# Kernel optimization log

Hardware: AMD Instinct MI355X
Metric: run time of the kernel (lower is better)

Reference implementation:

```python
import jax, jax.numpy as jnp
import numpy as np

D_MODEL = 1024
N_HEADS = 16
D_K = D_MODEL // N_HEADS


def setup_inputs() -> dict:
    key = jax.random.key(0)
    ks = jax.random.split(key, 9)
    s = 1.0 / np.sqrt(D_MODEL)
    x = jax.random.normal(ks[0], (4, 2048, D_MODEL), dtype=jnp.float32)
    def lin(kw, kb):
        W = jax.random.uniform(kw, (D_MODEL, D_MODEL), jnp.float32, -s, s)
        b = jax.random.uniform(kb, (D_MODEL,), jnp.float32, -s, s)
        return W, b
    w_q, b_q = lin(ks[1], ks[2])
    w_k, b_k = lin(ks[3], ks[4])
    w_v, b_v = lin(ks[5], ks[6])
    w_o, b_o = lin(ks[7], ks[8])
    return {"x": x, "w_q": w_q, "b_q": b_q, "w_k": w_k, "b_k": b_k,
            "w_v": w_v, "b_v": b_v, "w_o": w_o, "b_o": b_o}


def reference(x, w_q, b_q, w_k, b_k, w_v, b_v, w_o, b_o):
    B, S, _ = x.shape
    # projections; nn.Linear computes x @ W^T + b, here W stored as [in, out]
    def proj(W, b):
        return (x @ W + b).reshape(B, S, N_HEADS, D_K).transpose(0, 2, 1, 3)  # [B,H,S,Dk]
    q = proj(w_q, b_q)
    k = proj(w_k, b_k)
    v = proj(w_v, b_v)
    scores = jnp.einsum("bhsd,bhtd->bhst", q, k) / jnp.sqrt(jnp.float32(D_K))
    attn = jax.nn.softmax(scores, axis=-1)  # dropout p=0 -> identity
    ctx = jnp.einsum("bhst,bhtd->bhsd", attn, v)
    ctx = ctx.transpose(0, 2, 1, 3).reshape(B, S, D_MODEL)
    return ctx @ w_o + b_o
```

## Files before the change

### kernel.cpp

```cpp
#include <hip/hip_runtime.h>
#include <stdint.h>

typedef __attribute__((ext_vector_type(8))) short bf8;
typedef __attribute__((ext_vector_type(4))) float f4;
typedef __attribute__((ext_vector_type(16))) float f16v;
typedef __attribute__((ext_vector_type(4))) int i4;
typedef __attribute__((ext_vector_type(2))) int i2;
typedef unsigned short u16;

#define LDK 56

#define GLOAD16(gptr, lptr)                                                        \
    __builtin_amdgcn_global_load_lds((const __attribute__((address_space(1))) void*)(gptr), \
                                     (__attribute__((address_space(3))) void*)(lptr), 16, 0, 0)

static __device__ inline u16 f2bfbits(float f) {
    unsigned u = __float_as_uint(f);
    unsigned r = 0x7FFFu + ((u >> 16) & 1u);
    return (u16)((u + r) >> 16);
}

static __device__ inline int cvtpk(float lo, float hi) {
    int r;
    asm("v_cvt_pk_bf16_f32 %0, %1, %2" : "=v"(r) : "v"(lo), "v"(hi));
    return r;
}

__global__ void cvt_bf16(const float* __restrict__ in, u16* __restrict__ out, int n) {
    int i = (blockIdx.x * 256 + threadIdx.x) * 4;
    if (i < n) {
        float4 v = *(const float4*)(in + i);
        ushort4 o;
        o.x = f2bfbits(v.x); o.y = f2bfbits(v.y);
        o.z = f2bfbits(v.z); o.w = f2bfbits(v.w);
        *(ushort4*)(out + i) = o;
    }
}

__global__ void transpose4(const float* __restrict__ w0, const float* __restrict__ w1,
                           const float* __restrict__ w2, const float* __restrict__ w3,
                           u16* __restrict__ o0, u16* __restrict__ o1,
                           u16* __restrict__ o2, u16* __restrict__ o3) {
    __shared__ float tile[32][33];
    const float* w = blockIdx.z == 0 ? w0 : blockIdx.z == 1 ? w1 : blockIdx.z == 2 ? w2 : w3;
    u16* o = blockIdx.z == 0 ? o0 : blockIdx.z == 1 ? o1 : blockIdx.z == 2 ? o2 : o3;
    int bx = blockIdx.x * 32, by = blockIdx.y * 32;
    int tx = threadIdx.x, ty = threadIdx.y;
#pragma unroll
    for (int r = 0; r < 32; r += 8)
        tile[ty + r][tx] = w[(size_t)(by + ty + r) * 1024 + bx + tx];
    __syncthreads();
#pragma unroll
    for (int r = 0; r < 32; r += 8)
        o[(size_t)(bx + ty + r) * 1024 + by + tx] = f2bfbits(tile[tx][ty + r]);
}

__global__ __launch_bounds__(256) void gemm128(
    const u16* __restrict__ A, const u16* __restrict__ BT,
    const float* __restrict__ bias,
    u16* __restrict__ outb, float* __restrict__ outf, int mode) {
    __shared__ __align__(16) short As[128][LDK];
    __shared__ __align__(16) short Bs[128][LDK];
    const int tid = threadIdx.x;
    const int lane = tid & 63;
    const int l15 = lane & 15, lg = lane >> 4;
    const int wave = tid >> 6;
    const int wm = (wave >> 1) * 64, wn = (wave & 1) * 64;
    const int m0 = blockIdx.x * 128, n0 = blockIdx.y * 128;
    const int srow = tid >> 2;
    const int scol = (tid & 3) * 8;

    f4 acc[4][4] = {};

    for (int k0 = 0; k0 < 1024; k0 += 32) {
        bf8 a0 = *(const bf8*)(A + (size_t)(m0 + srow) * 1024 + k0 + scol);
        bf8 a1 = *(const bf8*)(A + (size_t)(m0 + srow + 64) * 1024 + k0 + scol);
        bf8 b0 = *(const bf8*)(BT + (size_t)(n0 + srow) * 1024 + k0 + scol);
        bf8 b1 = *(const bf8*)(BT + (size_t)(n0 + srow + 64) * 1024 + k0 + scol);
        __syncthreads();
        *(bf8*)(&As[srow][scol]) = a0;
        *(bf8*)(&As[srow + 64][scol]) = a1;
        *(bf8*)(&Bs[srow][scol]) = b0;
        *(bf8*)(&Bs[srow + 64][scol]) = b1;
        __syncthreads();
        bf8 af[4], bfr[4];
#pragma unroll
        for (int i = 0; i < 4; ++i) af[i] = *(const bf8*)(&As[wm + i * 16 + l15][lg * 8]);
#pragma unroll
        for (int j = 0; j < 4; ++j) bfr[j] = *(const bf8*)(&Bs[wn + j * 16 + l15][lg * 8]);
#pragma unroll
        for (int i = 0; i < 4; ++i)
#pragma unroll
            for (int j = 0; j < 4; ++j)
                acc[i][j] = __builtin_amdgcn_mfma_f32_16x16x32_bf16(af[i], bfr[j], acc[i][j], 0, 0, 0);
    }

    float bj[4];
#pragma unroll
    for (int j = 0; j < 4; ++j) bj[j] = bias[n0 + wn + j * 16 + l15];
    const float sc = (mode == 2) ? 0.125f * 1.44269504088896340736f : 1.0f;

    if (mode == 1) {
#pragma unroll
        for (int i = 0; i < 4; ++i) {
            int gm = m0 + wm + i * 16 + lg * 4;
#pragma unroll
            for (int j = 0; j < 4; ++j) {
                int gn = n0 + wn + j * 16 + l15;
#pragma unroll
                for (int r = 0; r < 4; ++r)
                    outf[(size_t)(gm + r) * 1024 + gn] = acc[i][j][r] + bj[j];
            }
        }
    } else if (mode == 3) {
#pragma unroll
        for (int i = 0; i < 4; ++i) {
            int gm = m0 + wm + i * 16 + lg * 4;
            int b_ = gm >> 11, s0 = gm & 2047;
#pragma unroll
            for (int j = 0; j < 4; ++j) {
                int gn = n0 + wn + j * 16 + l15;
                int h = gn >> 6, d = gn & 63;
                ushort4 w;
                w.x = f2bfbits(acc[i][j][0] + bj[j]);
                w.y = f2bfbits(acc[i][j][1] + bj[j]);
                w.z = f2bfbits(acc[i][j][2] + bj[j]);
                w.w = f2bfbits(acc[i][j][3] + bj[j]);
                *(ushort4*)(outb + ((size_t)(b_ * 16 + h) * 64 + d) * 2048 + s0) = w;
            }
        }
    } else {
#pragma unroll
        for (int i = 0; i < 4; ++i) {
            int gm = m0 + wm + i * 16 + lg * 4;
#pragma unroll
            for (int j = 0; j < 4; ++j) {
                int gn = n0 + wn + j * 16 + l15;
                int h = gn >> 6, d = gn & 63;
#pragma unroll
                for (int r = 0; r < 4; ++r) {
                    int m = gm + r;
                    int b_ = m >> 11, s = m & 2047;
                    float vv = (acc[i][j][r] + bj[j]) * sc;
                    outb[(((size_t)(b_ * 16 + h) * 2048) + s) * 64 + d] = f2bfbits(vv);
                }
            }
        }
    }
}

static __device__ inline void softmax_pv(f16v s, float& l,
                                         f16v& ocA, f16v& ocB, const bf8* vf) {
    float s0 = 0.f, s1 = 0.f, s2 = 0.f, s3 = 0.f;
#pragma unroll
    for (int r = 0; r < 16; r += 4) {
        s[r + 0] = __builtin_amdgcn_exp2f(s[r + 0]); s0 += s[r + 0];
        s[r + 1] = __builtin_amdgcn_exp2f(s[r + 1]); s1 += s[r + 1];
        s[r + 2] = __builtin_amdgcn_exp2f(s[r + 2]); s2 += s[r + 2];
        s[r + 3] = __builtin_amdgcn_exp2f(s[r + 3]); s3 += s[r + 3];
    }
    float ps = (s0 + s1) + (s2 + s3);
    {
        i2 sw = __builtin_amdgcn_permlane32_swap(__float_as_int(ps), __float_as_int(ps), false, false);
        ps = __int_as_float(sw[0]) + __int_as_float(sw[1]);
    }
    l += ps;

    i4 w0, w1;
    {
        i2 r0 = __builtin_amdgcn_permlane32_swap(cvtpk(s[0], s[1]),   cvtpk(s[4], s[5]),   false, false);
        i2 r1 = __builtin_amdgcn_permlane32_swap(cvtpk(s[2], s[3]),   cvtpk(s[6], s[7]),   false, false);
        i2 r2 = __builtin_amdgcn_permlane32_swap(cvtpk(s[8], s[9]),   cvtpk(s[12], s[13]), false, false);
        i2 r3 = __builtin_amdgcn_permlane32_swap(cvtpk(s[10], s[11]), cvtpk(s[14], s[15]), false, false);
        w0[0] = r0[0]; w0[1] = r1[0]; w0[2] = r0[1]; w0[3] = r1[1];
        w1[0] = r2[0]; w1[1] = r3[0]; w1[2] = r2[1]; w1[3] = r3[1];
    }
    union { i4 i; bf8 h; } pa0, pa1;
    pa0.i = w0; pa1.i = w1;

    __builtin_amdgcn_s_setprio(1);
    ocA = __builtin_amdgcn_mfma_f32_32x32x16_bf16(vf[0], pa0.h, ocA, 0, 0, 0);
    ocB = __builtin_amdgcn_mfma_f32_32x32x16_bf16(vf[2], pa0.h, ocB, 0, 0, 0);
    ocA = __builtin_amdgcn_mfma_f32_32x32x16_bf16(vf[1], pa1.h, ocA, 0, 0, 0);
    ocB = __builtin_amdgcn_mfma_f32_32x32x16_bf16(vf[3], pa1.h, ocB, 0, 0, 0);
    __builtin_amdgcn_s_setprio(0);
}

__global__ __launch_bounds__(256, 4) void attn(
    const u16* __restrict__ Q, const u16* __restrict__ K, const u16* __restrict__ VT,
    u16* __restrict__ ctx) {
    __shared__ __align__(16) char Kl[2][8192];
    __shared__ __align__(16) char Vl[2][8192];

    const int tid = threadIdx.x;
    const int lane = tid & 63, wave = tid >> 6;
    const int l31 = lane & 31, hi = lane >> 5;

    const int g = blockIdx.x;
    const int xcd = g & 7, li = g >> 3;
    const int bh = xcd * 8 + (li >> 4);
    const int qblk = li & 15;
    const int q0 = qblk * 128 + wave * 32;

    const char* Kg = (const char*)(K + (size_t)bh * 2048 * 64);
    const char* Vg = (const char*)(VT + (size_t)bh * 64 * 2048);

    const int p0 = wave * 1024 + lane * 16;
    const int p1 = p0 + 4096;
    const int r0 = p0 >> 7, r1 = p1 >> 7;
    const int sc0 = (p0 & 127) ^ ((r0 & 7) << 4);
    const int sc1 = (p1 & 127) ^ ((r1 & 7) << 4);

    GLOAD16(Kg + (size_t)r0 * 128 + sc0, &Kl[0][wave * 1024]);
    GLOAD16(Kg + (size_t)r1 * 128 + sc1, &Kl[0][4096 + wave * 1024]);
    GLOAD16(Vg + (size_t)r0 * 4096 + sc0, &Vl[0][wave * 1024]);
    GLOAD16(Vg + (size_t)r1 * 4096 + sc1, &Vl[0][4096 + wave * 1024]);

    bf8 qf[4];
    {
        const u16* Qr = Q + ((size_t)bh * 2048 + q0 + l31) * 64 + hi * 8;
#pragma unroll
        for (int c = 0; c < 4; ++c) qf[c] = *(const bf8*)(Qr + c * 16);
    }

    f16v oc0 = {}, oc1 = {};
    float l = 0.f;
    const int sw = (l31 & 7) << 4;

    __syncthreads();

    int cur = 0;
    for (int it = 0; it < 32; ++it) {
        const int t0 = it * 64;
        if (it + 1 < 32) {
            const int nxt = cur ^ 1;
            const size_t tn = (size_t)(t0 + 64);
            GLOAD16(Kg + (tn + r0) * 128 + sc0, &Kl[nxt][wave * 1024]);
            GLOAD16(Kg + (tn + r1) * 128 + sc1, &Kl[nxt][4096 + wave * 1024]);
            GLOAD16(Vg + (size_t)r0 * 4096 + tn * 2 + sc0, &Vl[nxt][wave * 1024]);
            GLOAD16(Vg + (size_t)r1 * 4096 + tn * 2 + sc1, &Vl[nxt][4096 + wave * 1024]);
        }
        const char* Kb = Kl[cur];
        const char* Vb = Vl[cur];

#pragma unroll
        for (int st = 0; st < 2; ++st) {
            bf8 kf[4];
#pragma unroll
            for (int c = 0; c < 4; ++c)
                kf[c] = *(const bf8*)(Kb + (st * 32 + l31) * 128 + ((c * 32 + hi * 16) ^ sw));

            f16v s;
#pragma unroll
            for (int r = 0; r < 16; ++r) s[r] = -10.f;
            __builtin_amdgcn_s_setprio(1);
#pragma unroll
            for (int c = 0; c < 4; ++c)
                s = __builtin_amdgcn_mfma_f32_32x32x16_bf16(kf[c], qf[c], s, 0, 0, 0);
            __builtin_amdgcn_s_setprio(0);

            bf8 vf[4];
#pragma unroll
            for (int dt = 0; dt < 2; ++dt)
#pragma unroll
                for (int tc = 0; tc < 2; ++tc)
                    vf[dt * 2 + tc] = *(const bf8*)(Vb + (dt * 32 + l31) * 128 +
                                                    ((st * 64 + tc * 32 + hi * 16) ^ sw));

            softmax_pv(s, l, oc0, oc1, vf);
        }
        __syncthreads();
        cur ^= 1;
    }

    const int b_ = bh >> 4, hd = bh & 15;
    const float rl = __builtin_amdgcn_rcpf(l);
    u16* Cr = ctx + ((size_t)(b_ * 2048) + q0 + l31) * 1024 + hd * 64;
#pragma unroll
    for (int gi = 0; gi < 4; ++gi) {
        ushort4 w;
        w.x = f2bfbits(oc0[gi * 4 + 0] * rl);
        w.y = f2bfbits(oc0[gi * 4 + 1] * rl);
        w.z = f2bfbits(oc0[gi * 4 + 2] * rl);
        w.w = f2bfbits(oc0[gi * 4 + 3] * rl);
        *(ushort4*)(Cr + gi * 8 + hi * 4) = w;
    }
#pragma unroll
    for (int gi = 0; gi < 4; ++gi) {
        ushort4 w;
        w.x = f2bfbits(oc1[gi * 4 + 0] * rl);
        w.y = f2bfbits(oc1[gi * 4 + 1] * rl);
        w.z = f2bfbits(oc1[gi * 4 + 2] * rl);
        w.w = f2bfbits(oc1[gi * 4 + 3] * rl);
        *(ushort4*)(Cr + 32 + gi * 8 + hi * 4) = w;
    }
}

extern "C" void kernel_launch(void* const* d_in, const int* in_sizes, int n_in,
                              void* d_out, int out_size, void* d_ws, size_t ws_size,
                              hipStream_t stream) {
    const float* x  = (const float*)d_in[0];
    const float* wq = (const float*)d_in[1];
    const float* bq = (const float*)d_in[2];
    const float* wk = (const float*)d_in[3];
    const float* bk = (const float*)d_in[4];
    const float* wv = (const float*)d_in[5];
    const float* bv = (const float*)d_in[6];
    const float* wo = (const float*)d_in[7];
    const float* bo = (const float*)d_in[8];
    float* out = (float*)d_out;

    char* ws = (char*)d_ws;
    u16* xb  = (u16*)ws;
    u16* wtq = (u16*)(ws + (size_t)(16 << 20));
    u16* wtk = wtq + 1024 * 1024;
    u16* wtv = wtk + 1024 * 1024;
    u16* wto = wtv + 1024 * 1024;
    u16* q   = (u16*)(ws + (size_t)(24 << 20));
    u16* k   = q + 8192 * 1024;
    u16* vt  = k + 8192 * 1024;
    u16* ctx = vt + 8192 * 1024;

    hipLaunchKernelGGL(cvt_bf16, dim3(8192), dim3(256), 0, stream, x, xb, 8192 * 1024);
    hipLaunchKernelGGL(transpose4, dim3(32, 32, 4), dim3(32, 8), 0, stream,
                       wq, wk, wv, wo, wtq, wtk, wtv, wto);
    dim3 gg(64, 8);
    hipLaunchKernelGGL(gemm128, gg, dim3(256), 0, stream, xb, wtq, bq, q,  (float*)nullptr, 2);
    hipLaunchKernelGGL(gemm128, gg, dim3(256), 0, stream, xb, wtk, bk, k,  (float*)nullptr, 0);
    hipLaunchKernelGGL(gemm128, gg, dim3(256), 0, stream, xb, wtv, bv, vt, (float*)nullptr, 3);
    hipLaunchKernelGGL(attn, dim3(1024), dim3(256), 0, stream, q, k, vt, ctx);
    hipLaunchKernelGGL(gemm128, gg, dim3(256), 0, stream, ctx, wto, bo, (u16*)nullptr, out, 1);
}
```

Before: 211.2 us.

## Fuse QKV projections into one GEMM launch with direct-to-LDS swizzled loads

Merges the three Q/K/V projection GEMMs into one launch over a 64x24 grid. This works because the transposed weights wtq/wtk/wtv sit next to each other in memory, so one BT pointer covers all three; bias and output routing are chosen from n0. The GEMM main loop now uses global_load_lds to stage tiles straight into LDS with an XOR swizzle instead of padded register round-trips. It also raises wave priority around the MFMA block. The aim is to cut launch overhead, register staging and LDS bank conflicts, at the cost of a single-buffered load that still waits on a barrier each k-step.

```diff
diff --git a/kernel.cpp b/kernel.cpp
--- a/kernel.cpp
+++ b/kernel.cpp
@@ -7,8 +7,6 @@
 typedef __attribute__((ext_vector_type(4))) int i4;
 typedef __attribute__((ext_vector_type(2))) int i2;
 typedef unsigned short u16;
-
-#define LDK 56
 
 #define GLOAD16(gptr, lptr)                                                        \
     __builtin_amdgcn_global_load_lds((const __attribute__((address_space(1))) void*)(gptr), \
@@ -55,96 +53,124 @@
         o[(size_t)(bx + ty + r) * 1024 + by + tx] = f2bfbits(tile[tx][ty + r]);
 }
 
-__global__ __launch_bounds__(256) void gemm128(
+#define GEMM_MAINLOOP(A_, B_, m0_, n0_)                                              \
+    const int tid = threadIdx.x;                                                     \
+    const int lane = tid & 63;                                                       \
+    const int l15 = lane & 15, lg = lane >> 4;                                       \
+    const int wave = tid >> 6;                                                       \
+    const int wm = (wave >> 1) * 64, wn = (wave & 1) * 64;                           \
+    const int sr = wave * 16 + (lane >> 2);       \
+    const int sc = lane & 3;                                      \
+    f4 acc[4][4] = {};                                                               \
+    for (int k0 = 0; k0 < 1024; k0 += 32) {                                          \
+        _Pragma("unroll")                                                            \
+        for (int j = 0; j < 2; ++j) {                                                \
+            int r = j * 64 + sr;                                                     \
+            int c = sc ^ ((r >> 1) & 3);                                             \
+            GLOAD16(A_ + (size_t)(m0_ + r) * 1024 + k0 + c * 8,                      \
+                    Asl + j * 4096 + wave * 1024);                                   \
+            GLOAD16(B_ + (size_t)(n0_ + r) * 1024 + k0 + c * 8,                      \
+                    Bsl + j * 4096 + wave * 1024);                                   \
+        }                                                                            \
+        __syncthreads();                                                             \
+        bf8 af[4], bfr[4];                                                           \
+        _Pragma("unroll")                                                            \
+        for (int i = 0; i < 4; ++i) {                                                \
+            int r = wm + i * 16 + l15;                                               \
+            af[i] = *(const bf8*)(Asl + r * 64 + ((lg ^ ((r >> 1) & 3)) * 16));      \
+        }                                                                            \
+        _Pragma("unroll")                                                            \
+        for (int j = 0; j < 4; ++j) {                                                \
+            int r = wn + j * 16 + l15;                                               \
+            bfr[j] = *(const bf8*)(Bsl + r * 64 + ((lg ^ ((r >> 1) & 3)) * 16));     \
+        }                                                                            \
+        __builtin_amdgcn_s_setprio(1);                                               \
+        _Pragma("unroll")                                                            \
+        for (int i = 0; i < 4; ++i)                                                  \
+            _Pragma("unroll")                                                        \
+            for (int j = 0; j < 4; ++j)                                              \
+                acc[i][j] = __builtin_amdgcn_mfma_f32_16x16x32_bf16(af[i], bfr[j],   \
+                                                                    acc[i][j], 0, 0, 0); \
+        __builtin_amdgcn_s_setprio(0);                                               \
+        __syncthreads();                                                             \
+    }
+
+__global__ __launch_bounds__(256) void gemm_qkv(
     const u16* __restrict__ A, const u16* __restrict__ BT,
-    const float* __restrict__ bias,
-    u16* __restrict__ outb, float* __restrict__ outf, int mode) {
-    __shared__ __align__(16) short As[128][LDK];
-    __shared__ __align__(16) short Bs[128][LDK];
-    const int tid = threadIdx.x;
-    const int lane = tid & 63;
-    const int l15 = lane & 15, lg = lane >> 4;
-    const int wave = tid >> 6;
-    const int wm = (wave >> 1) * 64, wn = (wave & 1) * 64;
+    const float* __restrict__ bq, const float* __restrict__ bk, const float* __restrict__ bv,
+    u16* __restrict__ qo, u16* __restrict__ ko, u16* __restrict__ vo) {
+    __shared__ __align__(16) char Asl[8192];
+    __shared__ __align__(16) char Bsl[8192];
     const int m0 = blockIdx.x * 128, n0 = blockIdx.y * 128;
-    const int srow = tid >> 2;
-    const int scol = (tid & 3) * 8;
-
-    f4 acc[4][4] = {};
-
-    for (int k0 = 0; k0 < 1024; k0 += 32) {
-        bf8 a0 = *(const bf8*)(A + (size_t)(m0 + srow) * 1024 + k0 + scol);
-        bf8 a1 = *(const bf8*)(A + (size_t)(m0 + srow + 64) * 1024 + k0 + scol);
-        bf8 b0 = *(const bf8*)(BT + (size_t)(n0 + srow) * 1024 + k0 + scol);
-        bf8 b1 = *(const bf8*)(BT + (size_t)(n0 + srow + 64) * 1024 + k0 + scol);
-        __syncthreads();
-        *(bf8*)(&As[srow][scol]) = a0;
-        *(bf8*)(&As[srow + 64][scol]) = a1;
-        *(bf8*)(&Bs[srow][scol]) = b0;
-        *(bf8*)(&Bs[srow + 64][scol]) = b1;
-        __syncthreads();
-        bf8 af[4], bfr[4];
-#pragma unroll
-        for (int i = 0; i < 4; ++i) af[i] = *(const bf8*)(&As[wm + i * 16 + l15][lg * 8]);
-#pragma unroll
-        for (int j = 0; j < 4; ++j) bfr[j] = *(const bf8*)(&Bs[wn + j * 16 + l15][lg * 8]);
-#pragma unroll
-        for (int i = 0; i < 4; ++i)
-#pragma unroll
-            for (int j = 0; j < 4; ++j)
-                acc[i][j] = __builtin_amdgcn_mfma_f32_16x16x32_bf16(af[i], bfr[j], acc[i][j], 0, 0, 0);
-    }
-
+
+    GEMM_MAINLOOP(A, BT, m0, n0)
+
+    const int reg = n0 >> 10;
+    const float* bp = reg == 0 ? bq : reg == 1 ? bk : bv;
+    const float scq = reg == 0 ? 0.125f * 1.44269504088896340736f : 1.0f;
     float bj[4];
 #pragma unroll
-    for (int j = 0; j < 4; ++j) bj[j] = bias[n0 + wn + j * 16 + l15];
-    const float sc = (mode == 2) ? 0.125f * 1.44269504088896340736f : 1.0f;
-
-    if (mode == 1) {
+    for (int j = 0; j < 4; ++j) bj[j] = bp[(n0 + wn + j * 16 + l15) & 1023];
+
+    if (reg < 2) {
+        u16* outb = reg == 0 ? qo : ko;
 #pragma unroll
         for (int i = 0; i < 4; ++i) {
             int gm = m0 + wm + i * 16 + lg * 4;
 #pragma unroll
             for (int j = 0; j < 4; ++j) {
-                int gn = n0 + wn + j * 16 + l15;
-#pragma unroll
-                for (int r = 0; r < 4; ++r)
-                    outf[(size_t)(gm + r) * 1024 + gn] = acc[i][j][r] + bj[j];
+                int gn = (n0 + wn + j * 16 + l15) & 1023;
+                int h = gn >> 6, d = gn & 63;
+#pragma unroll
+                for (int r = 0; r < 4; ++r) {
+                    int m = gm + r;
+                    int b_ = m >> 11, s = m & 2047;
+                    float vv = (acc[i][j][r] + bj[j]) * scq;
+                    outb[(((size_t)(b_ * 16 + h) * 2048) + s) * 64 + d] = f2bfbits(vv);
+                }
             }
         }
-    } else if (mode == 3) {
+    } else {
 #pragma unroll
         for (int i = 0; i < 4; ++i) {
             int gm = m0 + wm + i * 16 + lg * 4;
             int b_ = gm >> 11, s0 = gm & 2047;
 #pragma unroll
             for (int j = 0; j < 4; ++j) {
-                int gn = n0 + wn + j * 16 + l15;
+                int gn = (n0 + wn + j * 16 + l15) & 1023;
                 int h = gn >> 6, d = gn & 63;
                 ushort4 w;
                 w.x = f2bfbits(acc[i][j][0] + bj[j]);
                 w.y = f2bfbits(acc[i][j][1] + bj[j]);
                 w.z = f2bfbits(acc[i][j][2] + bj[j]);
                 w.w = f2bfbits(acc[i][j][3] + bj[j]);
-                *(ushort4*)(outb + ((size_t)(b_ * 16 + h) * 64 + d) * 2048 + s0) = w;
+                *(ushort4*)(vo + ((size_t)(b_ * 16 + h) * 64 + d) * 2048 + s0) = w;
             }
         }
-    } else {
-#pragma unroll
-        for (int i = 0; i < 4; ++i) {
-            int gm = m0 + wm + i * 16 + lg * 4;
-#pragma unroll
-            for (int j = 0; j < 4; ++j) {
-                int gn = n0 + wn + j * 16 + l15;
-                int h = gn >> 6, d = gn & 63;
-#pragma unroll
-                for (int r = 0; r < 4; ++r) {
-                    int m = gm + r;
-                    int b_ = m >> 11, s = m & 2047;
-                    float vv = (acc[i][j][r] + bj[j]) * sc;
-                    outb[(((size_t)(b_ * 16 + h) * 2048) + s) * 64 + d] = f2bfbits(vv);
-                }
-            }
+    }
+}
+
+__global__ __launch_bounds__(256) void gemm_o(
+    const u16* __restrict__ A, const u16* __restrict__ BT,
+    const float* __restrict__ bias, float* __restrict__ outf) {
+    __shared__ __align__(16) char Asl[8192];
+    __shared__ __align__(16) char Bsl[8192];
+    const int m0 = blockIdx.x * 128, n0 = blockIdx.y * 128;
+
+    GEMM_MAINLOOP(A, BT, m0, n0)
+
+    float bj[4];
+#pragma unroll
+    for (int j = 0; j < 4; ++j) bj[j] = bias[n0 + wn + j * 16 + l15];
+#pragma unroll
+    for (int i = 0; i < 4; ++i) {
+        int gm = m0 + wm + i * 16 + lg * 4;
+#pragma unroll
+        for (int j = 0; j < 4; ++j) {
+            int gn = n0 + wn + j * 16 + l15;
+#pragma unroll
+            for (int r = 0; r < 4; ++r)
+                outf[(size_t)(gm + r) * 1024 + gn] = acc[i][j][r] + bj[j];
         }
     }
 }
@@ -324,10 +350,8 @@
     hipLaunchKernelGGL(cvt_bf16, dim3(8192), dim3(256), 0, stream, x, xb, 8192 * 1024);
     hipLaunchKernelGGL(transpose4, dim3(32, 32, 4), dim3(32, 8), 0, stream,
                        wq, wk, wv, wo, wtq, wtk, wtv, wto);
-    dim3 gg(64, 8);
-    hipLaunchKernelGGL(gemm128, gg, dim3(256), 0, stream, xb, wtq, bq, q,  (float*)nullptr, 2);
-    hipLaunchKernelGGL(gemm128, gg, dim3(256), 0, stream, xb, wtk, bk, k,  (float*)nullptr, 0);
-    hipLaunchKernelGGL(gemm128, gg, dim3(256), 0, stream, xb, wtv, bv, vt, (float*)nullptr, 3);
+    hipLaunchKernelGGL(gemm_qkv, dim3(64, 24), dim3(256), 0, stream,
+                       xb, wtq, bq, bk, bv, q, k, vt);
     hipLaunchKernelGGL(attn, dim3(1024), dim3(256), 0, stream, q, k, vt, ctx);
-    hipLaunchKernelGGL(gemm128, gg, dim3(256), 0, stream, ctx, wto, bo, (u16*)nullptr, out, 1);
-}
+    hipLaunchKernelGGL(gemm_o, dim3(64, 8), dim3(256), 0, stream, ctx, wto, bo, out);
+}
```

Result: faster. 196.6 us (-6.9%).

## Pipeline GEMMs with async LDS loads, fuse QKV launches, unroll attention tile

Applied to the files above, without the earlier changes.

The register-staged GEMM with two syncs per k-step is replaced by a triple-buffered pipeline. It uses direct global-to-LDS loads into XOR-swizzled LDS, waits on vmcnt and raises MFMA priority. The three Q/K/V projection GEMMs become one launch over a 64x24 grid. This relies on the wq/wk/wv transposes being contiguous in the workspace so BT spans all three. The attention inner loop now processes both 32-key subtiles together, issuing the two QK MFMA chains and the softmax/PV work in one fused step to expose more ILP, at some register cost.

```diff
diff --git a/kernel.cpp b/kernel.cpp
--- a/kernel.cpp
+++ b/kernel.cpp
@@ -7,8 +7,6 @@
 typedef __attribute__((ext_vector_type(4))) int i4;
 typedef __attribute__((ext_vector_type(2))) int i2;
 typedef unsigned short u16;
-
-#define LDK 56
 
 #define GLOAD16(gptr, lptr)                                                        \
     __builtin_amdgcn_global_load_lds((const __attribute__((address_space(1))) void*)(gptr), \
@@ -55,134 +53,226 @@
         o[(size_t)(bx + ty + r) * 1024 + by + tx] = f2bfbits(tile[tx][ty + r]);
 }
 
-__global__ __launch_bounds__(256) void gemm128(
-    const u16* __restrict__ A, const u16* __restrict__ BT,
-    const float* __restrict__ bias,
-    u16* __restrict__ outb, float* __restrict__ outf, int mode) {
-    __shared__ __align__(16) short As[128][LDK];
-    __shared__ __align__(16) short Bs[128][LDK];
+static __device__ __attribute__((always_inline)) void gemm_pipe(
+    const u16* __restrict__ A_, const u16* __restrict__ B_, int m0, int n0,
+    char* Asl, char* Bsl, f4 (&acc)[4][4]) {
     const int tid = threadIdx.x;
     const int lane = tid & 63;
     const int l15 = lane & 15, lg = lane >> 4;
     const int wave = tid >> 6;
     const int wm = (wave >> 1) * 64, wn = (wave & 1) * 64;
-    const int m0 = blockIdx.x * 128, n0 = blockIdx.y * 128;
-    const int srow = tid >> 2;
-    const int scol = (tid & 3) * 8;
-
-    f4 acc[4][4] = {};
-
-    for (int k0 = 0; k0 < 1024; k0 += 32) {
-        bf8 a0 = *(const bf8*)(A + (size_t)(m0 + srow) * 1024 + k0 + scol);
-        bf8 a1 = *(const bf8*)(A + (size_t)(m0 + srow + 64) * 1024 + k0 + scol);
-        bf8 b0 = *(const bf8*)(BT + (size_t)(n0 + srow) * 1024 + k0 + scol);
-        bf8 b1 = *(const bf8*)(BT + (size_t)(n0 + srow + 64) * 1024 + k0 + scol);
-        __syncthreads();
-        *(bf8*)(&As[srow][scol]) = a0;
-        *(bf8*)(&As[srow + 64][scol]) = a1;
-        *(bf8*)(&Bs[srow][scol]) = b0;
-        *(bf8*)(&Bs[srow + 64][scol]) = b1;
-        __syncthreads();
+    const int sr = lane >> 2, sc = lane & 3;
+
+    const int rA0 = wave * 32 + sr;
+    const int rA1 = rA0 + 16;
+    const int cA0 = sc ^ ((rA0 >> 1) & 3);
+    const int cA1 = sc ^ ((rA1 >> 1) & 3);
+    const u16* pA0 = A_ + (size_t)(m0 + rA0) * 1024 + cA0 * 8;
+    const u16* pA1 = A_ + (size_t)(m0 + rA1) * 1024 + cA1 * 8;
+    const u16* pB0 = B_ + (size_t)(n0 + rA0) * 1024 + cA0 * 8;
+    const u16* pB1 = B_ + (size_t)(n0 + rA1) * 1024 + cA1 * 8;
+
+#pragma unroll
+    for (int p = 0; p < 3; ++p) {
+        const int k0 = p * 32;
+        GLOAD16(pA0 + k0, Asl + p * 8192 + wave * 2048);
+        GLOAD16(pA1 + k0, Asl + p * 8192 + wave * 2048 + 1024);
+        GLOAD16(pB0 + k0, Bsl + p * 8192 + wave * 2048);
+        GLOAD16(pB1 + k0, Bsl + p * 8192 + wave * 2048 + 1024);
+    }
+
+    int offA[4], offB[4];
+#pragma unroll
+    for (int i = 0; i < 4; ++i) {
+        int r = wm + i * 16 + l15;
+        offA[i] = r * 64 + ((lg ^ ((r >> 1) & 3)) * 16);
+    }
+#pragma unroll
+    for (int j = 0; j < 4; ++j) {
+        int r = wn + j * 16 + l15;
+        offB[j] = r * 64 + ((lg ^ ((r >> 1) & 3)) * 16);
+    }
+
+    int b = 0;
+    for (int kt = 0; kt < 32; ++kt) {
+        asm volatile("s_waitcnt vmcnt(8)" ::: "memory");
+        __builtin_amdgcn_s_barrier();
+        __builtin_amdgcn_sched_barrier(0);
+        const char* Ab = Asl + b * 8192;
+        const char* Bb = Bsl + b * 8192;
         bf8 af[4], bfr[4];
 #pragma unroll
-        for (int i = 0; i < 4; ++i) af[i] = *(const bf8*)(&As[wm + i * 16 + l15][lg * 8]);
-#pragma unroll
-        for (int j = 0; j < 4; ++j) bfr[j] = *(const bf8*)(&Bs[wn + j * 16 + l15][lg * 8]);
+        for (int i = 0; i < 4; ++i) af[i] = *(const bf8*)(Ab + offA[i]);
+#pragma unroll
+        for (int j = 0; j < 4; ++j) bfr[j] = *(const bf8*)(Bb + offB[j]);
+        asm volatile("s_waitcnt lgkmcnt(0)" ::: "memory");
+        __builtin_amdgcn_sched_barrier(0);
+        __builtin_amdgcn_s_setprio(1);
 #pragma unroll
         for (int i = 0; i < 4; ++i)
 #pragma unroll
             for (int j = 0; j < 4; ++j)
                 acc[i][j] = __builtin_amdgcn_mfma_f32_16x16x32_bf16(af[i], bfr[j], acc[i][j], 0, 0, 0);
-    }
-
+        __builtin_amdgcn_s_setprio(0);
+        __builtin_amdgcn_sched_barrier(0);
+        __builtin_amdgcn_s_barrier();
+        __builtin_amdgcn_sched_barrier(0);
+        {
+            const int k0 = ((kt + 3) & 31) * 32;
+            GLOAD16(pA0 + k0, Asl + b * 8192 + wave * 2048);
+            GLOAD16(pA1 + k0, Asl + b * 8192 + wave * 2048 + 1024);
+            GLOAD16(pB0 + k0, Bsl + b * 8192 + wave * 2048);
+            GLOAD16(pB1 + k0, Bsl + b * 8192 + wave * 2048 + 1024);
+        }
+        b = (b == 2) ? 0 : b + 1;
+    }
+    asm volatile("s_waitcnt vmcnt(0)" ::: "memory");
+}
+
+__global__ __launch_bounds__(256, 3) void gemm_qkv(
+    const u16* __restrict__ A, const u16* __restrict__ BT,
+    const float* __restrict__ bq, const float* __restrict__ bk, const float* __restrict__ bv,
+    u16* __restrict__ qo, u16* __restrict__ ko, u16* __restrict__ vo) {
+    __shared__ __align__(16) char Asl[24576];
+    __shared__ __align__(16) char Bsl[24576];
+    const int m0 = blockIdx.x * 128, n0 = blockIdx.y * 128;
+    f4 acc[4][4] = {};
+    gemm_pipe(A, BT, m0, n0, Asl, Bsl, acc);
+
+    const int lane = threadIdx.x & 63;
+    const int l15 = lane & 15, lg = lane >> 4;
+    const int wave = threadIdx.x >> 6;
+    const int wm = (wave >> 1) * 64, wn = (wave & 1) * 64;
+
+    const int reg = n0 >> 10;
+    const float* bp = reg == 0 ? bq : reg == 1 ? bk : bv;
+    const float scq = reg == 0 ? 0.125f * 1.44269504088896340736f : 1.0f;
     float bj[4];
 #pragma unroll
-    for (int j = 0; j < 4; ++j) bj[j] = bias[n0 + wn + j * 16 + l15];
-    const float sc = (mode == 2) ? 0.125f * 1.44269504088896340736f : 1.0f;
-
-    if (mode == 1) {
+    for (int j = 0; j < 4; ++j) bj[j] = bp[(n0 + wn + j * 16 + l15) & 1023];
+
+    if (reg < 2) {
+        u16* outb = reg == 0 ? qo : ko;
 #pragma unroll
         for (int i = 0; i < 4; ++i) {
             int gm = m0 + wm + i * 16 + lg * 4;
 #pragma unroll
             for (int j = 0; j < 4; ++j) {
-                int gn = n0 + wn + j * 16 + l15;
-#pragma unroll
-                for (int r = 0; r < 4; ++r)
-                    outf[(size_t)(gm + r) * 1024 + gn] = acc[i][j][r] + bj[j];
+                int gn = (n0 + wn + j * 16 + l15) & 1023;
+                int h = gn >> 6, d = gn & 63;
+#pragma unroll
+                for (int r = 0; r < 4; ++r) {
+                    int m = gm + r;
+                    int b_ = m >> 11, s = m & 2047;
+                    float vv = (acc[i][j][r] + bj[j]) * scq;
+                    outb[(((size_t)(b_ * 16 + h) * 2048) + s) * 64 + d] = f2bfbits(vv);
+                }
             }
         }
-    } else if (mode == 3) {
+    } else {
 #pragma unroll
         for (int i = 0; i < 4; ++i) {
             int gm = m0 + wm + i * 16 + lg * 4;
             int b_ = gm >> 11, s0 = gm & 2047;
 #pragma unroll
             for (int j = 0; j < 4; ++j) {
-                int gn = n0 + wn + j * 16 + l15;
+                int gn = (n0 + wn + j * 16 + l15) & 1023;
                 int h = gn >> 6, d = gn & 63;
                 ushort4 w;
                 w.x = f2bfbits(acc[i][j][0] + bj[j]);
                 w.y = f2bfbits(acc[i][j][1] + bj[j]);
                 w.z = f2bfbits(acc[i][j][2] + bj[j]);
                 w.w = f2bfbits(acc[i][j][3] + bj[j]);
-                *(ushort4*)(outb + ((size_t)(b_ * 16 + h) * 64 + d) * 2048 + s0) = w;
+                *(ushort4*)(vo + ((size_t)(b_ * 16 + h) * 64 + d) * 2048 + s0) = w;
             }
         }
-    } else {
-#pragma unroll
-        for (int i = 0; i < 4; ++i) {
-            int gm = m0 + wm + i * 16 + lg * 4;
-#pragma unroll
-            for (int j = 0; j < 4; ++j) {
-                int gn = n0 + wn + j * 16 + l15;
-                int h = gn >> 6, d = gn & 63;
-#pragma unroll
-                for (int r = 0; r < 4; ++r) {
-                    int m = gm + r;
-                    int b_ = m >> 11, s = m & 2047;
-                    float vv = (acc[i][j][r] + bj[j]) * sc;
-                    outb[(((size_t)(b_ * 16 + h) * 2048) + s) * 64 + d] = f2bfbits(vv);
-                }
-            }
-        }
-    }
-}
-
-static __device__ inline void softmax_pv(f16v s, float& l,
-                                         f16v& ocA, f16v& ocB, const bf8* vf) {
-    float s0 = 0.f, s1 = 0.f, s2 = 0.f, s3 = 0.f;
+    }
+}
+
+__global__ __launch_bounds__(256, 3) void gemm_o(
+    const u16* __restrict__ A, const u16* __restrict__ BT,
+    const float* __restrict__ bias, float* __restrict__ outf) {
+    __shared__ __align__(16) char Asl[24576];
+    __shared__ __align__(16) char Bsl[24576];
+    const int m0 = blockIdx.x * 128, n0 = blockIdx.y * 128;
+    f4 acc[4][4] = {};
+    gemm_pipe(A, BT, m0, n0, Asl, Bsl, acc);
+
+    const int lane = threadIdx.x & 63;
+    const int l15 = lane & 15, lg = lane >> 4;
+    const int wave = threadIdx.x >> 6;
+    const int wm = (wave >> 1) * 64, wn = (wave & 1) * 64;
+
+    float bj[4];
+#pragma unroll
+    for (int j = 0; j < 4; ++j) bj[j] = bias[n0 + wn + j * 16 + l15];
+#pragma unroll
+    for (int i = 0; i < 4; ++i) {
+        int gm = m0 + wm + i * 16 + lg * 4;
+#pragma unroll
+        for (int j = 0; j < 4; ++j) {
+            int gn = n0 + wn + j * 16 + l15;
+#pragma unroll
+            for (int r = 0; r < 4; ++r)
+                outf[(size_t)(gm + r) * 1024 + gn] = acc[i][j][r] + bj[j];
+        }
+    }
+}
+
+static __device__ inline void softmax_pv2(f16v sa, f16v sb, float& l,
+                                          f16v& oc0, f16v& oc1,
+                                          const bf8* vfa, const bf8* vfb) {
+    float t0 = 0.f, t1 = 0.f, t2 = 0.f, t3 = 0.f;
 #pragma unroll
     for (int r = 0; r < 16; r += 4) {
-        s[r + 0] = __builtin_amdgcn_exp2f(s[r + 0]); s0 += s[r + 0];
-        s[r + 1] = __builtin_amdgcn_exp2f(s[r + 1]); s1 += s[r + 1];
-        s[r + 2] = __builtin_amdgcn_exp2f(s[r + 2]); s2 += s[r + 2];
-        s[r + 3] = __builtin_amdgcn_exp2f(s[r + 3]); s3 += s[r + 3];
-    }
-    float ps = (s0 + s1) + (s2 + s3);
+        sa[r + 0] = __builtin_amdgcn_exp2f(sa[r + 0]); t0 += sa[r + 0];
+        sa[r + 1] = __builtin_amdgcn_exp2f(sa[r + 1]); t1 += sa[r + 1];
+        sa[r + 2] = __builtin_amdgcn_exp2f(sa[r + 2]); t2 += sa[r + 2];
+        sa[r + 3] = __builtin_amdgcn_exp2f(sa[r + 3]); t3 += sa[r + 3];
+    }
+#pragma unroll
+    for (int r = 0; r < 16; r += 4) {
+        sb[r + 0] = __builtin_amdgcn_exp2f(sb[r + 0]); t0 += sb[r + 0];
+        sb[r + 1] = __builtin_amdgcn_exp2f(sb[r + 1]); t1 += sb[r + 1];
+        sb[r + 2] = __builtin_amdgcn_exp2f(sb[r + 2]); t2 += sb[r + 2];
+        sb[r + 3] = __builtin_amdgcn_exp2f(sb[r + 3]); t3 += sb[r + 3];
+    }
+    float ps = (t0 + t1) + (t2 + t3);
     {
         i2 sw = __builtin_amdgcn_permlane32_swap(__float_as_int(ps), __float_as_int(ps), false, false);
         ps = __int_as_float(sw[0]) + __int_as_float(sw[1]);
     }
     l += ps;
 
-    i4 w0, w1;
+    i4 w0a, w1a, w0b, w1b;
     {
-        i2 r0 = __builtin_amdgcn_permlane32_swap(cvtpk(s[0], s[1]),   cvtpk(s[4], s[5]),   false, false);
-        i2 r1 = __builtin_amdgcn_permlane32_swap(cvtpk(s[2], s[3]),   cvtpk(s[6], s[7]),   false, false);
-        i2 r2 = __builtin_amdgcn_permlane32_swap(cvtpk(s[8], s[9]),   cvtpk(s[12], s[13]), false, false);
-        i2 r3 = __builtin_amdgcn_permlane32_swap(cvtpk(s[10], s[11]), cvtpk(s[14], s[15]), false, false);
-        w0[0] = r0[0]; w0[1] = r1[0]; w0[2] = r0[1]; w0[3] = r1[1];
-        w1[0] = r2[0]; w1[1] = r3[0]; w1[2] = r2[1]; w1[3] = r3[1];
-    }
-    union { i4 i; bf8 h; } pa0, pa1;
-    pa0.i = w0; pa1.i = w1;
+        i2 r0 = __builtin_amdgcn_permlane32_swap(cvtpk(sa[0], sa[1]),   cvtpk(sa[4], sa[5]),   false, false);
+        i2 r1 = __builtin_amdgcn_permlane32_swap(cvtpk(sa[2], sa[3]),   cvtpk(sa[6], sa[7]),   false, false);
+        i2 r2 = __builtin_amdgcn_permlane32_swap(cvtpk(sa[8], sa[9]),   cvtpk(sa[12], sa[13]), false, false);
+        i2 r3 = __builtin_amdgcn_permlane32_swap(cvtpk(sa[10], sa[11]), cvtpk(sa[14], sa[15]), false, false);
+        w0a[0] = r0[0]; w0a[1] = r1[0]; w0a[2] = r0[1]; w0a[3] = r1[1];
+        w1a[0] = r2[0]; w1a[1] = r3[0]; w1a[2] = r2[1]; w1a[3] = r3[1];
+    }
+    {
+        i2 r0 = __builtin_amdgcn_permlane32_swap(cvtpk(sb[0], sb[1]),   cvtpk(sb[4], sb[5]),   false, false);
+        i2 r1 = __builtin_amdgcn_permlane32_swap(cvtpk(sb[2], sb[3]),   cvtpk(sb[6], sb[7]),   false, false);
+        i2 r2 = __builtin_amdgcn_permlane32_swap(cvtpk(sb[8], sb[9]),   cvtpk(sb[12], sb[13]), false, false);
+        i2 r3 = __builtin_amdgcn_permlane32_swap(cvtpk(sb[10], sb[11]), cvtpk(sb[14], sb[15]), false, false);
+        w0b[0] = r0[0]; w0b[1] = r1[0]; w0b[2] = r0[1]; w0b[3] = r1[1];
+        w1b[0] = r2[0]; w1b[1] = r3[0]; w1b[2] = r2[1]; w1b[3] = r3[1];
+    }
+    union { i4 i; bf8 h; } pa0, pa1, pb0, pb1;
+    pa0.i = w0a; pa1.i = w1a; pb0.i = w0b; pb1.i = w1b;
 
     __builtin_amdgcn_s_setprio(1);
-    ocA = __builtin_amdgcn_mfma_f32_32x32x16_bf16(vf[0], pa0.h, ocA, 0, 0, 0);
-    ocB = __builtin_amdgcn_mfma_f32_32x32x16_bf16(vf[2], pa0.h, ocB, 0, 0, 0);
-    ocA = __builtin_amdgcn_mfma_f32_32x32x16_bf16(vf[1], pa1.h, ocA, 0, 0, 0);
-    ocB = __builtin_amdgcn_mfma_f32_32x32x16_bf16(vf[3], pa1.h, ocB, 0, 0, 0);
+    oc0 = __builtin_amdgcn_mfma_f32_32x32x16_bf16(vfa[0], pa0.h, oc0, 0, 0, 0);
+    oc1 = __builtin_amdgcn_mfma_f32_32x32x16_bf16(vfa[2], pa0.h, oc1, 0, 0, 0);
+    oc0 = __builtin_amdgcn_mfma_f32_32x32x16_bf16(vfa[1], pa1.h, oc0, 0, 0, 0);
+    oc1 = __builtin_amdgcn_mfma_f32_32x32x16_bf16(vfa[3], pa1.h, oc1, 0, 0, 0);
+    oc0 = __builtin_amdgcn_mfma_f32_32x32x16_bf16(vfb[0], pb0.h, oc0, 0, 0, 0);
+    oc1 = __builtin_amdgcn_mfma_f32_32x32x16_bf16(vfb[2], pb0.h, oc1, 0, 0, 0);
+    oc0 = __builtin_amdgcn_mfma_f32_32x32x16_bf16(vfb[1], pb1.h, oc0, 0, 0, 0);
+    oc1 = __builtin_amdgcn_mfma_f32_32x32x16_bf16(vfb[3], pb1.h, oc1, 0, 0, 0);
     __builtin_amdgcn_s_setprio(0);
 }
 
@@ -243,32 +333,37 @@
         const char* Kb = Kl[cur];
         const char* Vb = Vl[cur];
 
-#pragma unroll
-        for (int st = 0; st < 2; ++st) {
-            bf8 kf[4];
-#pragma unroll
-            for (int c = 0; c < 4; ++c)
-                kf[c] = *(const bf8*)(Kb + (st * 32 + l31) * 128 + ((c * 32 + hi * 16) ^ sw));
-
-            f16v s;
-#pragma unroll
-            for (int r = 0; r < 16; ++r) s[r] = -10.f;
-            __builtin_amdgcn_s_setprio(1);
-#pragma unroll
-            for (int c = 0; c < 4; ++c)
-                s = __builtin_amdgcn_mfma_f32_32x32x16_bf16(kf[c], qf[c], s, 0, 0, 0);
-            __builtin_amdgcn_s_setprio(0);
-
-            bf8 vf[4];
-#pragma unroll
-            for (int dt = 0; dt < 2; ++dt)
-#pragma unroll
-                for (int tc = 0; tc < 2; ++tc)
-                    vf[dt * 2 + tc] = *(const bf8*)(Vb + (dt * 32 + l31) * 128 +
-                                                    ((st * 64 + tc * 32 + hi * 16) ^ sw));
-
-            softmax_pv(s, l, oc0, oc1, vf);
-        }
+        bf8 kfa[4], kfb[4];
+#pragma unroll
+        for (int c = 0; c < 4; ++c) {
+            kfa[c] = *(const bf8*)(Kb + (l31) * 128 + ((c * 32 + hi * 16) ^ sw));
+            kfb[c] = *(const bf8*)(Kb + (32 + l31) * 128 + ((c * 32 + hi * 16) ^ sw));
+        }
+
+        f16v sa, sb;
+#pragma unroll
+        for (int r = 0; r < 16; ++r) { sa[r] = -10.f; sb[r] = -10.f; }
+        __builtin_amdgcn_s_setprio(1);
+#pragma unroll
+        for (int c = 0; c < 4; ++c) {
+            sa = __builtin_amdgcn_mfma_f32_32x32x16_bf16(kfa[c], qf[c], sa, 0, 0, 0);
+            sb = __builtin_amdgcn_mfma_f32_32x32x16_bf16(kfb[c], qf[c], sb, 0, 0, 0);
+        }
+        __builtin_amdgcn_s_setprio(0);
+
+        bf8 vfa[4], vfb[4];
+#pragma unroll
+        for (int dt = 0; dt < 2; ++dt)
+#pragma unroll
+            for (int tc = 0; tc < 2; ++tc) {
+                vfa[dt * 2 + tc] = *(const bf8*)(Vb + (dt * 32 + l31) * 128 +
+                                                ((tc * 32 + hi * 16) ^ sw));
+                vfb[dt * 2 + tc] = *(const bf8*)(Vb + (dt * 32 + l31) * 128 +
+                                                ((64 + tc * 32 + hi * 16) ^ sw));
+            }
+
+        softmax_pv2(sa, sb, l, oc0, oc1, vfa, vfb);
+
         __syncthreads();
         cur ^= 1;
     }
@@ -324,10 +419,8 @@
     hipLaunchKernelGGL(cvt_bf16, dim3(8192), dim3(256), 0, stream, x, xb, 8192 * 1024);
     hipLaunchKernelGGL(transpose4, dim3(32, 32, 4), dim3(32, 8), 0, stream,
                        wq, wk, wv, wo, wtq, wtk, wtv, wto);
-    dim3 gg(64, 8);
-    hipLaunchKernelGGL(gemm128, gg, dim3(256), 0, stream, xb, wtq, bq, q,  (float*)nullptr, 2);
-    hipLaunchKernelGGL(gemm128, gg, dim3(256), 0, stream, xb, wtk, bk, k,  (float*)nullptr, 0);
-    hipLaunchKernelGGL(gemm128, gg, dim3(256), 0, stream, xb, wtv, bv, vt, (float*)nullptr, 3);
+    hipLaunchKernelGGL(gemm_qkv, dim3(64, 24), dim3(256), 0, stream,
+                       xb, wtq, bq, bk, bv, q, k, vt);
     hipLaunchKernelGGL(attn, dim3(1024), dim3(256), 0, stream, q, k, vt, ctx);
-    hipLaunchKernelGGL(gemm128, gg, dim3(256), 0, stream, ctx, wto, bo, (u16*)nullptr, out, 1);
-}
+    hipLaunchKernelGGL(gemm_o, dim3(64, 8), dim3(256), 0, stream, ctx, wto, bo, out);
+}
```

Measured after the change: 321.6 us. 52.3% more time.
